# Kernel optimization log

Hardware: AMD Instinct MI355X
Metric: run time of the kernel (lower is better)

Reference implementation:

```python
import jax, jax.numpy as jnp
import numpy as np
import math

B, S, E, H, DK = 2, 2048, 1024, 16, 64  # batch, seq, embed, heads, d_k (= n_wires)

def setup_inputs() -> dict:
    key = jax.random.key(0)
    k1, k2, k3, k4, k5 = jax.random.split(key, 5)
    scale = 0.02
    return {
        "x": jax.random.normal(k1, (B, S, E), dtype=jnp.float32),
        "Wk": jax.random.normal(k2, (E, E), dtype=jnp.float32) * scale,
        "Wv": jax.random.normal(k3, (E, E), dtype=jnp.float32) * scale,
        "Wq": jax.random.normal(k4, (H, DK, E), dtype=jnp.float32) * scale,
        "theta": jax.random.normal(k5, (DK,), dtype=jnp.float32) * scale,
    }

def reference(x, Wk, Wv, Wq, theta):
    batch, seq, embed = x.shape
    n_heads, d_k = Wq.shape[0], Wq.shape[1]
    # K, V projections (nn.Linear, no bias): x @ W.T
    k = (x @ Wk.T).reshape(batch, seq, n_heads, d_k).transpose(0, 2, 1, 3)  # [B,H,S,dk]
    v = (x @ Wv.T).reshape(batch, seq, n_heads, d_k).transpose(0, 2, 1, 3)  # [B,H,S,dk]
    # Quantum query path: per-head linear proj -> RX(proj_i) then RX(theta_i) on wire i from |0>,
    # MeasureAll(PauliZ) on independent wires gives <Z_i> = cos(proj_i + theta_i) exactly.
    proj = jnp.einsum('bse,hde->bhsd', x, Wq)          # [B,H,S,dk]
    q = jnp.cos(proj + theta)                           # [B,H,S,dk]
    scores = jnp.einsum('bhsd,bhtd->bhst', q, k) / math.sqrt(d_k)  # [B,H,S,S]
    attn = jax.nn.softmax(scores, axis=-1)
    out = jnp.einsum('bhst,bhtd->bhsd', attn, v)        # [B,H,S,dk]
    return out.transpose(0, 2, 1, 3).reshape(batch, seq, embed)
```

## Files before the change

kernel.cpp:

```cpp
#include <hip/hip_runtime.h>
#include <hip/hip_bf16.h>

constexpr int B  = 2;
constexpr int S  = 2048;
constexpr int E  = 1024;
constexpr int H  = 16;
constexpr int DK = 64;
constexpr int M  = B * S;
constexpr int N3 = 3 * E;
constexpr long RSZ = (long)B * H * S * DK;

using bf16x8 = __attribute__((ext_vector_type(8))) __bf16;
using bf16x4 = __attribute__((ext_vector_type(4))) __bf16;
using f32x4  = __attribute__((ext_vector_type(4))) float;

__device__ __forceinline__ void async16(__bf16* lds, const __bf16* g) {
    __builtin_amdgcn_global_load_lds(
        (const __attribute__((address_space(1))) void*)g,
        (__attribute__((address_space(3))) void*)lds, 16, 0, 0);
}

__global__ __launch_bounds__(256)
void cvt_kernel(const float* __restrict__ x, const float* __restrict__ Wk,
                const float* __restrict__ Wv, const float* __restrict__ Wq,
                __bf16* __restrict__ xb, __bf16* __restrict__ wall) {
    const long e = ((long)blockIdx.x * 256 + threadIdx.x) * 4;
    const float* src;
    __bf16* dst;
    if (e < (long)M * E) { src = x + e; dst = xb + e; }
    else {
        const long e2 = e - (long)M * E;
        const int which = (int)(e2 >> 20);
        const long off  = e2 & ((1L << 20) - 1);
        src = (which == 0 ? Wk : which == 1 ? Wv : Wq) + off;
        dst = wall + e2;
    }
    float4 f = *reinterpret_cast<const float4*>(src);
    bf16x4 o;
    o[0] = (__bf16)f.x; o[1] = (__bf16)f.y; o[2] = (__bf16)f.z; o[3] = (__bf16)f.w;
    *reinterpret_cast<bf16x4*>(dst) = o;
}

__global__ __launch_bounds__(256, 3)
void qkv_gemm(const __bf16* __restrict__ xb, const __bf16* __restrict__ wall,
              const float* __restrict__ theta, __bf16* __restrict__ kvq) {
    __shared__ __align__(1024) __bf16 smem[4 * 128 * 32];
    __bf16* tile = smem;

    const int t    = threadIdx.x;
    const int lane = t & 63;
    const int w    = t >> 6;
    const int quad = lane >> 4;
    const int l16  = lane & 15;
    const int wm   = w >> 1, wn = w & 1;
    const int mbase = blockIdx.y * 128;
    const int nbase = blockIdx.x * 128;

    f32x4 acc[4][4];
    #pragma unroll
    for (int i = 0; i < 4; i++)
        #pragma unroll
        for (int j = 0; j < 4; j++)
            acc[i][j] = f32x4{0.f, 0.f, 0.f, 0.f};

    const int srow = lane >> 2;
    const int srcc = (lane & 3) ^ ((lane >> 3) & 3);
    const __bf16* ga = xb   + (long)(mbase + srow) * E + srcc * 8;
    const __bf16* gb = wall + (long)(nbase + srow) * E + srcc * 8;

    const int csw = (l16 >> 1) & 3;

    #pragma unroll
    for (int c = 0; c < 2; c++) {
        async16(smem +        (c * 64 + w * 16) * 32, ga + (long)(c * 64 + w * 16) * E);
        async16(smem + 8192 + (c * 64 + w * 16) * 32, gb + (long)(c * 64 + w * 16) * E);
    }

    for (int it = 0; it < E / 32; it++) {
        const int cur = it & 1;
        __syncthreads();

        if (it + 1 < E / 32) {
            const int kk1 = (it + 1) * 32;
            #pragma unroll
            for (int c = 0; c < 2; c++) {
                async16(smem + (cur ^ 1) * 4096 +        (c * 64 + w * 16) * 32,
                        ga + (long)(c * 64 + w * 16) * E + kk1);
                async16(smem + (cur ^ 1) * 4096 + 8192 + (c * 64 + w * 16) * 32,
                        gb + (long)(c * 64 + w * 16) * E + kk1);
            }
        }

        const __bf16* Asb = smem + cur * 4096;
        const __bf16* Bsb = smem + cur * 4096 + 8192;
        bf16x8 a[4], b[4];
        #pragma unroll
        for (int i = 0; i < 4; i++)
            a[i] = *reinterpret_cast<const bf16x8*>(
                &Asb[(wm * 64 + i * 16 + l16) * 32 + (quad ^ csw) * 8]);
        #pragma unroll
        for (int j = 0; j < 4; j++)
            b[j] = *reinterpret_cast<const bf16x8*>(
                &Bsb[(wn * 64 + j * 16 + l16) * 32 + (quad ^ csw) * 8]);
        #pragma unroll
        for (int i = 0; i < 4; i++)
            #pragma unroll
            for (int j = 0; j < 4; j++)
                acc[i][j] = __builtin_amdgcn_mfma_f32_16x16x32_bf16(a[i], b[j], acc[i][j], 0, 0, 0);
    }

    const int region = nbase >> 10;
    const int bb = mbase >> 11;
    if (region == 1) {
        __syncthreads();
        #pragma unroll
        for (int i = 0; i < 4; i++) {
            const int cchunk = wm * 8 + i * 2 + (quad >> 1);
            #pragma unroll
            for (int j = 0; j < 4; j++) {
                const int cirb = wn * 64 + j * 16 + l16;
                const int cs = cchunk ^ l16;
                bf16x4 pk;
                #pragma unroll
                for (int r = 0; r < 4; r++) pk[r] = (__bf16)acc[i][j][r];
                *reinterpret_cast<bf16x4*>(&tile[cirb * 128 + cs * 8 + (quad & 1) * 4]) = pk;
            }
        }
        __syncthreads();
        const int h0 = (nbase & 1023) >> 6;
        __bf16* vt = kvq + RSZ;
        #pragma unroll
        for (int p = 0; p < 8; p++) {
            const int dcol = p * 16 + (t >> 4);
            const int lc = t & 15;
            const int cs2 = lc ^ (dcol & 15);
            bf16x8 vv = *reinterpret_cast<const bf16x8*>(&tile[dcol * 128 + cs2 * 8]);
            const int hh = h0 + (dcol >> 6), d = dcol & 63;
            *reinterpret_cast<bf16x8*>(
                &vt[((long)(bb * H + hh) * DK + d) * S + (mbase & 2047) + lc * 8]) = vv;
        }
    } else {
        __bf16* dst = kvq + (region == 2 ? 2 * RSZ : 0);
        float th[4];
        if (region == 2) {
            #pragma unroll
            for (int j = 0; j < 4; j++) th[j] = theta[j * 16 + l16];
        }
        #pragma unroll
        for (int i = 0; i < 4; i++) {
            const int row0 = mbase + wm * 64 + i * 16 + quad * 4;
            #pragma unroll
            for (int j = 0; j < 4; j++) {
                const int cir = (nbase & 1023) + wn * 64 + j * 16 + l16;
                const int h = cir >> 6, d = cir & 63;
                #pragma unroll
                for (int r = 0; r < 4; r++) {
                    const int s = (row0 + r) & 2047;
                    float v = acc[i][j][r];
                    if (region == 2) v = cosf(v + th[j]) * 0.125f;
                    dst[((long)(bb * H + h) * S + s) * DK + d] = (__bf16)v;
                }
            }
        }
    }
}

__global__ __launch_bounds__(256, 2)
void attn_kernel(const __bf16* __restrict__ q_ws, const __bf16* __restrict__ k_ws,
                 const __bf16* __restrict__ v_ws, float* __restrict__ out) {
    __shared__ __align__(1024) __bf16 Ks[2][32 * 64];
    __shared__ __align__(1024) __bf16 Vs[2][64 * 32];
    __shared__ __align__(16)   __bf16 Pl[4][32 * 40];
    __shared__ __align__(16)   float  ls_lds[4][32];

    const int lane = threadIdx.x & 63;
    const int w    = threadIdx.x >> 6;
    const int quad = lane >> 4;
    const int l16  = lane & 15;

    const int id    = blockIdx.x;
    const int bh    = (id & 7) + 8 * ((id >> 3) & 3);
    const int qbase = (id >> 5) * 128 + w * 32;

    const __bf16* qp = q_ws + (long)bh * S * DK;
    const __bf16* kp = k_ws + (long)bh * S * DK;
    const __bf16* vp = v_ws + (long)bh * DK * S;

    const int ksr = lane >> 3, ksc = (lane & 7) ^ (lane >> 3);
    const int vsr = lane >> 2, vsc = (lane & 3) ^ ((lane >> 2) & 3);

    bf16x8 bq[2][2];
    #pragma unroll
    for (int nt = 0; nt < 2; nt++)
        #pragma unroll
        for (int ks = 0; ks < 2; ks++)
            bq[nt][ks] = *reinterpret_cast<const bf16x8*>(
                qp + (long)(qbase + nt * 16 + l16) * DK + ks * 32 + quad * 8);

    f32x4 o[2][4];
    #pragma unroll
    for (int i = 0; i < 2; i++)
        #pragma unroll
        for (int j = 0; j < 4; j++) o[i][j] = f32x4{0.f, 0.f, 0.f, 0.f};
    float lsum[2] = {0.f, 0.f};

    async16(&Ks[0][(w * 8) * 64],  kp + (long)(w * 8 + ksr) * DK + ksc * 8);
    async16(&Vs[0][(w * 16) * 32], vp + (long)(w * 16 + vsr) * S + vsc * 8);

    for (int it = 0; it < S / 32; it++) {
        const int cur = it & 1;
        __syncthreads();

        if (it + 1 < S / 32) {
            const int kt1 = (it + 1) * 32;
            async16(&Ks[cur ^ 1][(w * 8) * 64],
                    kp + (long)(kt1 + w * 8 + ksr) * DK + ksc * 8);
            async16(&Vs[cur ^ 1][(w * 16) * 32],
                    vp + (long)(w * 16 + vsr) * S + kt1 + vsc * 8);
        }

        f32x4 sacc[2][2];
        #pragma unroll
        for (int i = 0; i < 2; i++)
            #pragma unroll
            for (int j = 0; j < 2; j++) sacc[i][j] = f32x4{0.f, 0.f, 0.f, 0.f};
        #pragma unroll
        for (int ks = 0; ks < 2; ks++) {
            bf16x8 ak[2];
            #pragma unroll
            for (int mt = 0; mt < 2; mt++)
                ak[mt] = *reinterpret_cast<const bf16x8*>(
                    &Ks[cur][(mt * 16 + l16) * 64 + ((ks * 4 + quad) ^ (l16 & 7)) * 8]);
            #pragma unroll
            for (int mt = 0; mt < 2; mt++)
                #pragma unroll
                for (int nt = 0; nt < 2; nt++)
                    sacc[mt][nt] = __builtin_amdgcn_mfma_f32_16x16x32_bf16(
                        ak[mt], bq[nt][ks], sacc[mt][nt], 0, 0, 0);
        }

        #pragma unroll
        for (int mt = 0; mt < 2; mt++)
            #pragma unroll
            for (int nt = 0; nt < 2; nt++) {
                float p0 = __expf(sacc[mt][nt][0]);
                float p1 = __expf(sacc[mt][nt][1]);
                float p2 = __expf(sacc[mt][nt][2]);
                float p3 = __expf(sacc[mt][nt][3]);
                lsum[nt] += (p0 + p1) + (p2 + p3);
                bf16x4 pk;
                pk[0] = (__bf16)p0; pk[1] = (__bf16)p1;
                pk[2] = (__bf16)p2; pk[3] = (__bf16)p3;
                *reinterpret_cast<bf16x4*>(
                    &Pl[w][(nt * 16 + l16) * 40 + mt * 16 + quad * 4]) = pk;
            }

        #pragma unroll
        for (int mt = 0; mt < 2; mt++) {
            bf16x8 ap = *reinterpret_cast<const bf16x8*>(
                &Pl[w][(mt * 16 + l16) * 40 + quad * 8]);
            #pragma unroll
            for (int nt = 0; nt < 4; nt++) {
                bf16x8 bv = *reinterpret_cast<const bf16x8*>(
                    &Vs[cur][(nt * 16 + l16) * 32 + (quad ^ (l16 & 3)) * 8]);
                o[mt][nt] = __builtin_amdgcn_mfma_f32_16x16x32_bf16(ap, bv, o[mt][nt], 0, 0, 0);
            }
        }
    }

    #pragma unroll
    for (int nt = 0; nt < 2; nt++) {
        float v = lsum[nt];
        v += __shfl_xor(v, 16);
        v += __shfl_xor(v, 32);
        ls_lds[w][nt * 16 + l16] = v;
    }

    const int b = bh >> 4, h = bh & 15;
    #pragma unroll
    for (int mt = 0; mt < 2; mt++) {
        f32x4 lv = *reinterpret_cast<const f32x4*>(&ls_lds[w][mt * 16 + quad * 4]);
        #pragma unroll
        for (int r = 0; r < 4; r++) {
            const float inv = 1.0f / lv[r];
            const int srow = qbase + mt * 16 + quad * 4 + r;
            #pragma unroll
            for (int nt = 0; nt < 4; nt++)
                out[(long)(b * S + srow) * E + h * DK + nt * 16 + l16] = o[mt][nt][r] * inv;
        }
    }
}

__device__ inline bf16x8 cvt_frag(const float* __restrict__ p) {
    float4 f0 = *reinterpret_cast<const float4*>(p);
    float4 f1 = *reinterpret_cast<const float4*>(p + 4);
    bf16x8 r;
    r[0] = (__bf16)f0.x; r[1] = (__bf16)f0.y; r[2] = (__bf16)f0.z; r[3] = (__bf16)f0.w;
    r[4] = (__bf16)f1.x; r[5] = (__bf16)f1.y; r[6] = (__bf16)f1.z; r[7] = (__bf16)f1.w;
    return r;
}
template <int MODE>
__global__ __launch_bounds__(256, 2)
void proj_kernel(const float* __restrict__ x, const float* __restrict__ W,
                 const float* __restrict__ theta, __bf16* __restrict__ out) {
    const int lane = threadIdx.x & 63;
    const int w    = threadIdx.x >> 6;
    const int quad = lane >> 4;
    const int l16  = lane & 15;
    const int mbase = blockIdx.y * 128 + w * 32;
    const int nbase = blockIdx.x * 128;
    f32x4 acc[2][8];
    #pragma unroll
    for (int i = 0; i < 2; i++)
        #pragma unroll
        for (int j = 0; j < 8; j++) acc[i][j] = f32x4{0.f, 0.f, 0.f, 0.f};
    float th[4];
    if (MODE == 2) {
        #pragma unroll
        for (int j = 0; j < 4; j++) th[j] = theta[j * 16 + l16];
    }
    for (int kk = 0; kk < E; kk += 32) {
        bf16x8 a[2], b[8];
        #pragma unroll
        for (int mt = 0; mt < 2; mt++)
            a[mt] = cvt_frag(x + (long)(mbase + mt * 16 + l16) * E + kk + quad * 8);
        #pragma unroll
        for (int nt = 0; nt < 8; nt++)
            b[nt] = cvt_frag(W + (long)(nbase + nt * 16 + l16) * E + kk + quad * 8);
        #pragma unroll
        for (int mt = 0; mt < 2; mt++)
            #pragma unroll
            for (int nt = 0; nt < 8; nt++)
                acc[mt][nt] = __builtin_amdgcn_mfma_f32_16x16x32_bf16(a[mt], b[nt], acc[mt][nt], 0, 0, 0);
    }
    #pragma unroll
    for (int mt = 0; mt < 2; mt++) {
        const int row0 = mbase + mt * 16 + quad * 4;
        #pragma unroll
        for (int nt = 0; nt < 8; nt++) {
            const int col = nbase + nt * 16 + l16;
            const int h = col >> 6, d = col & 63;
            #pragma unroll
            for (int r = 0; r < 4; r++) {
                const int row = row0 + r;
                const int bb = row >> 11, s = row & 2047;
                float v = acc[mt][nt][r];
                if (MODE == 2) v = cosf(v + th[nt & 3]) * 0.125f;
                long idx;
                if (MODE == 1) idx = ((long)(bb * H + h) * DK + d) * S + s;
                else           idx = ((long)(bb * H + h) * S + s) * DK + d;
                out[idx] = (__bf16)v;
            }
        }
    }
}

extern "C" void kernel_launch(void* const* d_in, const int* in_sizes, int n_in,
                              void* d_out, int out_size, void* d_ws, size_t ws_size,
                              hipStream_t stream) {
    const float* x     = (const float*)d_in[0];
    const float* Wk    = (const float*)d_in[1];
    const float* Wv    = (const float*)d_in[2];
    const float* Wq    = (const float*)d_in[3];
    const float* theta = (const float*)d_in[4];
    float* out = (float*)d_out;

    __bf16* kvq  = (__bf16*)d_ws;
    __bf16* xb   = kvq + 3 * RSZ;
    __bf16* wall = xb + (long)M * E;
    __bf16* k_ws = kvq;
    __bf16* v_t  = kvq + RSZ;
    __bf16* q_ws = kvq + 2 * RSZ;

    const size_t need = (3 * RSZ + (long)M * E + (long)N3 * E) * 2;
    dim3 blk(256);
    if (ws_size >= need) {
        cvt_kernel<<<dim3(7168), blk, 0, stream>>>(x, Wk, Wv, Wq, xb, wall);
        qkv_gemm<<<dim3(N3 / 128, M / 128), blk, 0, stream>>>(xb, wall, theta, kvq);
    } else {
        dim3 gp(E / 128, M / 128);
        proj_kernel<0><<<gp, blk, 0, stream>>>(x, Wk, nullptr, k_ws);
        proj_kernel<1><<<gp, blk, 0, stream>>>(x, Wv, nullptr, v_t);
        proj_kernel<2><<<gp, blk, 0, stream>>>(x, Wq, theta, q_ws);
    }

    attn_kernel<<<dim3(512), blk, 0, stream>>>(q_ws, k_ws, v_t, out);
}
```

Measured before the change: 177.3 us.

## Triple-buffer LDS tiles with explicit vmcnt waits in GEMM and attention

Both the QKV GEMM and the attention kernel move from double to triple buffering of their LDS tiles and prefetch two tiles ahead instead of one. __syncthreads is replaced by a partial s_waitcnt vmcnt plus s_barrier, so the current tile's async loads are waited on while the next tile's loads stay in flight. This aims to hide more global-load latency. It costs more LDS per block, which could limit occupancy, and the hand-written vmcnt counts are fragile if the compiler emits extra loads.

```diff
diff --git a/kernel.cpp b/kernel.cpp
--- a/kernel.cpp
+++ b/kernel.cpp
@@ -44,7 +44,7 @@
 __global__ __launch_bounds__(256, 3)
 void qkv_gemm(const __bf16* __restrict__ xb, const __bf16* __restrict__ wall,
               const float* __restrict__ theta, __bf16* __restrict__ kvq) {
-    __shared__ __align__(1024) __bf16 smem[4 * 128 * 32];
+    __shared__ __align__(1024) __bf16 smem[6 * 128 * 32];
     __bf16* tile = smem;
 
     const int t    = threadIdx.x;
@@ -71,28 +71,37 @@
     const int csw = (l16 >> 1) & 3;
 
     #pragma unroll
-    for (int c = 0; c < 2; c++) {
-        async16(smem +        (c * 64 + w * 16) * 32, ga + (long)(c * 64 + w * 16) * E);
-        async16(smem + 8192 + (c * 64 + w * 16) * 32, gb + (long)(c * 64 + w * 16) * E);
-    }
-
-    for (int it = 0; it < E / 32; it++) {
-        const int cur = it & 1;
-        __syncthreads();
-
-        if (it + 1 < E / 32) {
-            const int kk1 = (it + 1) * 32;
+    for (int pt = 0; pt < 2; pt++) {
+        #pragma unroll
+        for (int c = 0; c < 2; c++) {
+            async16(smem + pt * 4096 +         (c * 64 + w * 16) * 32,
+                    ga + (long)(c * 64 + w * 16) * E + pt * 32);
+            async16(smem + pt * 4096 + 12288 + (c * 64 + w * 16) * 32,
+                    gb + (long)(c * 64 + w * 16) * E + pt * 32);
+        }
+    }
+
+    int cur = 0;
+    constexpr int ITERS = E / 32;
+    for (int it = 0; it < ITERS; it++) {
+        if (it < ITERS - 1) asm volatile("s_waitcnt vmcnt(4)" ::: "memory");
+        else                asm volatile("s_waitcnt vmcnt(0)" ::: "memory");
+        asm volatile("s_barrier" ::: "memory");
+
+        if (it + 2 < ITERS) {
+            const int pb  = (cur == 0) ? 2 : cur - 1;
+            const int kk2 = (it + 2) * 32;
             #pragma unroll
             for (int c = 0; c < 2; c++) {
-                async16(smem + (cur ^ 1) * 4096 +        (c * 64 + w * 16) * 32,
-                        ga + (long)(c * 64 + w * 16) * E + kk1);
-                async16(smem + (cur ^ 1) * 4096 + 8192 + (c * 64 + w * 16) * 32,
-                        gb + (long)(c * 64 + w * 16) * E + kk1);
+                async16(smem + pb * 4096 +         (c * 64 + w * 16) * 32,
+                        ga + (long)(c * 64 + w * 16) * E + kk2);
+                async16(smem + pb * 4096 + 12288 + (c * 64 + w * 16) * 32,
+                        gb + (long)(c * 64 + w * 16) * E + kk2);
             }
         }
 
         const __bf16* Asb = smem + cur * 4096;
-        const __bf16* Bsb = smem + cur * 4096 + 8192;
+        const __bf16* Bsb = smem + cur * 4096 + 12288;
         bf16x8 a[4], b[4];
         #pragma unroll
         for (int i = 0; i < 4; i++)
@@ -107,6 +116,8 @@
             #pragma unroll
             for (int j = 0; j < 4; j++)
                 acc[i][j] = __builtin_amdgcn_mfma_f32_16x16x32_bf16(a[i], b[j], acc[i][j], 0, 0, 0);
+
+        cur = (cur == 2) ? 0 : cur + 1;
     }
 
     const int region = nbase >> 10;
@@ -168,8 +179,8 @@
 __global__ __launch_bounds__(256, 2)
 void attn_kernel(const __bf16* __restrict__ q_ws, const __bf16* __restrict__ k_ws,
                  const __bf16* __restrict__ v_ws, float* __restrict__ out) {
-    __shared__ __align__(1024) __bf16 Ks[2][32 * 64];
-    __shared__ __align__(1024) __bf16 Vs[2][64 * 32];
+    __shared__ __align__(1024) __bf16 Ks[3][32 * 64];
+    __shared__ __align__(1024) __bf16 Vs[3][64 * 32];
     __shared__ __align__(16)   __bf16 Pl[4][32 * 40];
     __shared__ __align__(16)   float  ls_lds[4][32];
 
@@ -204,19 +215,26 @@
         for (int j = 0; j < 4; j++) o[i][j] = f32x4{0.f, 0.f, 0.f, 0.f};
     float lsum[2] = {0.f, 0.f};
 
-    async16(&Ks[0][(w * 8) * 64],  kp + (long)(w * 8 + ksr) * DK + ksc * 8);
-    async16(&Vs[0][(w * 16) * 32], vp + (long)(w * 16 + vsr) * S + vsc * 8);
-
-    for (int it = 0; it < S / 32; it++) {
-        const int cur = it & 1;
-        __syncthreads();
-
-        if (it + 1 < S / 32) {
-            const int kt1 = (it + 1) * 32;
-            async16(&Ks[cur ^ 1][(w * 8) * 64],
-                    kp + (long)(kt1 + w * 8 + ksr) * DK + ksc * 8);
-            async16(&Vs[cur ^ 1][(w * 16) * 32],
-                    vp + (long)(w * 16 + vsr) * S + kt1 + vsc * 8);
+    #pragma unroll
+    for (int pt = 0; pt < 2; pt++) {
+        async16(&Ks[pt][(w * 8) * 64],  kp + (long)(pt * 32 + w * 8 + ksr) * DK + ksc * 8);
+        async16(&Vs[pt][(w * 16) * 32], vp + (long)(w * 16 + vsr) * S + pt * 32 + vsc * 8);
+    }
+
+    int cur = 0;
+    constexpr int ITERS = S / 32;
+    for (int it = 0; it < ITERS; it++) {
+        if (it < ITERS - 1) asm volatile("s_waitcnt vmcnt(2)" ::: "memory");
+        else                asm volatile("s_waitcnt vmcnt(0)" ::: "memory");
+        asm volatile("s_barrier" ::: "memory");
+
+        if (it + 2 < ITERS) {
+            const int pb  = (cur == 0) ? 2 : cur - 1;
+            const int kt2 = (it + 2) * 32;
+            async16(&Ks[pb][(w * 8) * 64],
+                    kp + (long)(kt2 + w * 8 + ksr) * DK + ksc * 8);
+            async16(&Vs[pb][(w * 16) * 32],
+                    vp + (long)(w * 16 + vsr) * S + kt2 + vsc * 8);
         }
 
         f32x4 sacc[2][2];
@@ -266,6 +284,8 @@
                 o[mt][nt] = __builtin_amdgcn_mfma_f32_16x16x32_bf16(ap, bv, o[mt][nt], 0, 0, 0);
             }
         }
+
+        cur = (cur == 2) ? 0 : cur + 1;
     }
 
     #pragma unroll
```

Result: slower. 184.0 us (+3.8%).
